# Kernel optimization log

Hardware: AMD Instinct MI355X
Metric: run time of the kernel (lower is better)

## Reference

```python
import jax, jax.numpy as jnp
import numpy as np
import math

B, S, D = 2, 2048, 512
N_BUCKETS = 64
N_HYP = int(math.log2(N_BUCKETS))  # 6


def setup_inputs() -> dict:
    key = jax.random.key(0)
    ks = jax.random.split(key, 6)
    x = jax.random.normal(ks[0], (B, S, D), dtype=jnp.float32)
    # torch.nn.Linear params: weight [out,in], bias [out]
    Wq = jax.random.normal(ks[1], (D, D), dtype=jnp.float32) / jnp.sqrt(D)
    bq = jax.random.normal(ks[2], (D,), dtype=jnp.float32) * 0.01
    Wv = jax.random.normal(ks[3], (D, D), dtype=jnp.float32) / jnp.sqrt(D)
    bv = jax.random.normal(ks[4], (D,), dtype=jnp.float32) * 0.01
    hyperplanes = jax.random.normal(ks[5], (D + 1, N_HYP), dtype=jnp.float32)
    return {"x": x, "Wq": Wq, "bq": bq, "Wv": Wv, "bv": bv, "hyperplanes": hyperplanes}


def _get_buckets(q, hyperplanes):
    # append constant-1 feature: [B,S,D+1]
    qa = jnp.concatenate([q, jnp.ones(q.shape[:2] + (1,), q.dtype)], axis=2)
    proj = jnp.einsum('bse,en->bsn', qa, hyperplanes)
    bits = (proj >= 0).astype(jnp.float32)
    powers = (2.0 ** jnp.arange(N_HYP)).astype(jnp.float32)
    return jnp.einsum('bsn,n->bs', bits, powers)  # [B,S] float bucket ids


def reference(x, Wq, bq, Wv, bv, hyperplanes):
    q = x @ Wq.T + bq
    v = x @ Wv.T + bv
    buckets = _get_buckets(q, hyperplanes)  # [B,S]
    scale = 1.0 / math.sqrt(D)

    def body(acc, i):
        # NOTE: faithful to source: tokens IN bucket i are zeroed (masked_fill
        # with mask = buckets == i), then full dense softmax attention.
        mask = (buckets == i)[..., None]  # [B,S,1]
        qb = jnp.where(mask, 0.0, q)
        vb = jnp.where(mask, 0.0, v)
        att = jax.nn.softmax(jnp.einsum('bsd,btd->bst', qb, qb) * scale, axis=-1)
        return acc + jnp.einsum('bst,btd->bsd', att, vb), None

    init = jnp.zeros_like(x)
    out, _ = jax.lax.scan(body, init, jnp.arange(N_BUCKETS, dtype=jnp.float32))
    return out
```

## Files before the change

kernel.cpp:

```cpp
#include <hip/hip_runtime.h>
#include <math.h>

#define B_ 2
#define S_ 2048
#define D_ 512
#define NB_ 64
#define NH_ 6
#define ROWS (B_*S_)
#define SCALE 0.044194173824159216f

typedef float f32x4 __attribute__((ext_vector_type(4)));
typedef __bf16 bf16v8 __attribute__((ext_vector_type(8)));
typedef short s16x8 __attribute__((ext_vector_type(8)));
typedef unsigned short u16x4 __attribute__((ext_vector_type(4)));

__device__ __forceinline__ float b2f(unsigned short u) {
    unsigned int v = (unsigned int)u << 16;
    float f; __builtin_memcpy(&f, &v, 4); return f;
}
__device__ __forceinline__ unsigned short f2b(float f) {
    unsigned int v; __builtin_memcpy(&v, &f, 4);
    v += 0x7fffu + ((v >> 16) & 1u);
    return (unsigned short)(v >> 16);
}

#define GLOAD16(g, l) __builtin_amdgcn_global_load_lds( \
    (const __attribute__((address_space(1))) unsigned int*)(g), \
    (__attribute__((address_space(3))) unsigned int*)(uintptr_t)(l), 16, 0, 0)

__device__ __forceinline__ void stage_rows(
    const unsigned short* __restrict__ src, int r0, int k0, int ld,
    unsigned short* lds, int chunk0, int nch, int l)
{
    #pragma unroll
    for (int j = 0; j < nch; ++j) {
        int chunk = chunk0 + j;
        int r = chunk * 8 + (l >> 3);
        int c = (l & 7) ^ (l >> 3);
        GLOAD16(src + (size_t)(r0 + r) * ld + k0 + c * 8, lds + chunk * 512);
    }
}

template<int EPI>
__global__ __launch_bounds__(256) void mfma_nt(
    const unsigned short* __restrict__ A, const unsigned short* __restrict__ B,
    int N, int K, long long zA, long long zB,
    float* __restrict__ Cf, long long zC,
    unsigned short* __restrict__ Ch, long long zCh,
    const float* __restrict__ e0, long long z0,
    const float* __restrict__ e1, long long z1,
    const int* __restrict__ ib, long long zi)
{
    __shared__ unsigned short Als[128 * 64];
    __shared__ unsigned short Bls[64 * 64];
    int tid = threadIdx.x;
    int w = tid >> 6, l = tid & 63;
    int wr = w >> 1, wc = w & 1;
    int zb = blockIdx.z;
    A += zb * zA;  B += zb * zB;

    int gx = gridDim.x;
    int nwg = gx * gridDim.y;
    int lin = blockIdx.y * gx + blockIdx.x;
    int qq = nwg >> 3;
    int wg = (lin & 7) * qq + (lin >> 3);
    int m0 = (wg / gx) * 128, n0 = (wg % gx) * 64;

    f32x4 acc[4][2] = {};
    int rl = l & 15, hi = l >> 4;

    for (int k0 = 0; k0 < K; k0 += 64) {
        stage_rows(A, m0, k0, K, Als, w * 4, 4, l);
        stage_rows(B, n0, k0, K, Bls, w * 2, 2, l);
        __syncthreads();
        bf16v8 af[4][2], bfr[2][2];
        const char* Ab = (const char*)Als;
        const char* Bb = (const char*)Bls;
        #pragma unroll
        for (int kk = 0; kk < 2; ++kk) {
            int kb = kk * 64 + hi * 16;
            #pragma unroll
            for (int f = 0; f < 4; ++f) {
                int ra = wr * 64 + f * 16 + rl;
                af[f][kk] = *(const bf16v8*)(Ab + ra * 128 + (kb ^ ((ra & 7) << 4)));
            }
            #pragma unroll
            for (int f = 0; f < 2; ++f) {
                int rb = wc * 32 + f * 16 + rl;
                bfr[f][kk] = *(const bf16v8*)(Bb + rb * 128 + (kb ^ ((rb & 7) << 4)));
            }
        }
        #pragma unroll
        for (int fm = 0; fm < 4; ++fm)
            #pragma unroll
            for (int fn = 0; fn < 2; ++fn)
                #pragma unroll
                for (int kk = 0; kk < 2; ++kk)
                    acc[fm][fn] = __builtin_amdgcn_mfma_f32_16x16x32_bf16(
                        af[fm][kk], bfr[fn][kk], acc[fm][fn], 0, 0, 0);
        __syncthreads();
    }

    if (EPI == 0) {
        #pragma unroll
        for (int fm = 0; fm < 4; ++fm)
            #pragma unroll
            for (int fn = 0; fn < 2; ++fn) {
                int col = n0 + wc * 32 + fn * 16 + rl;
                if (col < D_) {
                    float bs = e0[col];
                    #pragma unroll
                    for (int r = 0; r < 4; ++r) {
                        int row = m0 + wr * 64 + fm * 16 + hi * 4 + r;
                        float cv = acc[fm][fn][r] + bs;
                        Cf[(size_t)row * D_ + col] = cv;
                        Ch[(size_t)row * D_ + col] = f2b(cv);
                    }
                } else {
                    int c2 = col - D_;
                    float bs = e1[c2];
                    #pragma unroll
                    for (int r = 0; r < 4; ++r) {
                        int row = m0 + wr * 64 + fm * 16 + hi * 4 + r;
                        float cv = acc[fm][fn][r] + bs;
                        ((float*)ib)[(size_t)row * D_ + c2] = cv;
                    }
                }
            }
    } else if (EPI == 1) {
        Ch += zb * zCh;  e0 += zb * z0;
        #pragma unroll
        for (int fm = 0; fm < 4; ++fm)
            #pragma unroll
            for (int fn = 0; fn < 2; ++fn) {
                int col = n0 + wc * 32 + fn * 16 + rl;
                #pragma unroll
                for (int r = 0; r < 4; ++r) {
                    int row = m0 + wr * 64 + fm * 16 + hi * 4 + r;
                    float ev = __expf(fmaf(acc[fm][fn][r], SCALE, -e0[row]));
                    Ch[(size_t)row * N + col] = f2b(ev);
                }
            }
    } else {
        Cf += zb * zC;  e0 += zb * z0;  e1 += zb * z1;  ib += zb * zi;
        const float invS = 1.0f / (float)S_;
        #pragma unroll
        for (int fm = 0; fm < 4; ++fm)
            #pragma unroll
            for (int fn = 0; fn < 2; ++fn) {
                int col = n0 + wc * 32 + fn * 16 + rl;
                float sva = e0[col];
                #pragma unroll
                for (int r = 0; r < 4; ++r) {
                    int row = m0 + wr * 64 + fm * 16 + hi * 4 + r;
                    int bm = ib[row];
                    Cf[(size_t)row * N + col] =
                        acc[fm][fn][r] + (sva - e1[(size_t)bm * D_ + col]) * invS;
                }
            }
    }
}

__global__ void convert_bf16(const float* __restrict__ src, unsigned short* __restrict__ dst, int n)
{
    for (int i = (blockIdx.x * 256 + threadIdx.x) * 4; i < n; i += gridDim.x * 1024) {
        float4 f = *(const float4*)(src + i);
        u16x4 u = { f2b(f.x), f2b(f.y), f2b(f.z), f2b(f.w) };
        *(u16x4*)(dst + i) = u;
    }
}

__global__ __launch_bounds__(256) void transpose_v(
    const float* __restrict__ v, const int* __restrict__ perm,
    unsigned short* __restrict__ vT)
{
    __shared__ float tl[32][33];
    int b = blockIdx.z;
    int d0 = blockIdx.x * 32, s0 = blockIdx.y * 32;
    int tx = threadIdx.x & 31, ty = threadIdx.x >> 5;
    const float* vb = v + (size_t)b * S_ * D_;
    const int* pm = perm + (size_t)b * S_;
    #pragma unroll
    for (int i = 0; i < 4; ++i)
        tl[ty + i * 8][tx] = vb[(size_t)pm[s0 + ty + i * 8] * D_ + d0 + tx];
    __syncthreads();
    unsigned short* vt = vT + (size_t)b * D_ * S_;
    #pragma unroll
    for (int i = 0; i < 4; ++i)
        vt[(size_t)(d0 + ty + i * 8) * S_ + s0 + tx] = f2b(tl[tx][ty + i * 8]);
}

__global__ __launch_bounds__(64) void bucket_kernel(
    const float* __restrict__ q, const float* __restrict__ H,
    int* __restrict__ bucket, float* __restrict__ Mrow)
{
    int row = blockIdx.x;
    int lane = threadIdx.x;
    const float* qr = q + (size_t)row * D_;
    float proj[NH_] = {};
    float nrm = 0.f;
    for (int d = lane; d < D_; d += 64) {
        float qv = qr[d];
        float qb = b2f(f2b(qv));
        nrm = fmaf(qb, qb, nrm);
        #pragma unroll
        for (int n = 0; n < NH_; ++n)
            proj[n] = fmaf(qv, H[d * NH_ + n], proj[n]);
    }
    #pragma unroll
    for (int off = 32; off; off >>= 1) {
        nrm += __shfl_down(nrm, off);
        #pragma unroll
        for (int n = 0; n < NH_; ++n) proj[n] += __shfl_down(proj[n], off);
    }
    if (lane == 0) {
        int bk = 0;
        #pragma unroll
        for (int n = 0; n < NH_; ++n) {
            float p = proj[n] + H[D_ * NH_ + n];
            if (p >= 0.f) bk |= (1 << n);
        }
        bucket[row] = bk;
        Mrow[row] = nrm * SCALE;
    }
}

__global__ void zero_cnt(int* __restrict__ cnt) { cnt[threadIdx.x] = 0; }

__global__ __launch_bounds__(256) void hist_kernel(
    const int* __restrict__ bucket, int* __restrict__ cnt, int* __restrict__ idxl)
{
    int r = blockIdx.x * 256 + threadIdx.x;
    int b = r / S_;
    int s = r - b * S_;
    int j = bucket[r];
    int pos = atomicAdd(&cnt[b * NB_ + j], 1);
    idxl[((size_t)(b * NB_ + j)) * S_ + pos] = s;
}

__global__ __launch_bounds__(64) void prefix_kernel(
    const int* __restrict__ cnt, int* __restrict__ off)
{
    int b = blockIdx.x;
    int j = threadIdx.x;
    int c = cnt[b * NB_ + j];
    int x = c;
    #pragma unroll
    for (int o = 1; o < 64; o <<= 1) {
        int y = __shfl_up(x, o);
        if (j >= o) x += y;
    }
    off[b * (NB_ + 1) + j] = x - c;
    if (j == 63) off[b * (NB_ + 1) + 64] = x;
}

__global__ __launch_bounds__(64) void permbuild_kernel(
    const int* __restrict__ idxl, const int* __restrict__ cnt,
    const int* __restrict__ off, int* __restrict__ perm, int* __restrict__ p2b)
{
    int j = blockIdx.x, b = blockIdx.y;
    int n = cnt[b * NB_ + j];
    int o = off[b * (NB_ + 1) + j];
    const int* lst = idxl + ((size_t)(b * NB_ + j)) * S_;
    for (int k = threadIdx.x; k < n; k += 64) {
        perm[(size_t)b * S_ + o + k] = lst[k];
        p2b[(size_t)b * S_ + o + k] = j;
    }
}

__global__ __launch_bounds__(64) void gatherq_kernel(
    const unsigned short* __restrict__ qh, const int* __restrict__ perm,
    unsigned short* __restrict__ qp)
{
    int tp = blockIdx.x;
    int b = tp >> 11, tl = tp & (S_ - 1);
    int src = perm[(size_t)b * S_ + tl];
    const unsigned short* sp = qh + ((size_t)b * S_ + src) * D_;
    unsigned short* dp = qp + (size_t)tp * D_;
    int t = threadIdx.x * 8;
    *(s16x8*)(dp + t) = *(const s16x8*)(sp + t);
}

__global__ __launch_bounds__(256) void zwgamma_kernel(
    unsigned short* __restrict__ Eh, const int* __restrict__ p2b,
    const int* __restrict__ off, const int* __restrict__ cnt,
    const int* __restrict__ bucket, const float* __restrict__ Mrow)
{
    int row = blockIdx.x;
    int b = row >> 11;
    __shared__ float er[S_];
    __shared__ float zl[NB_];
    __shared__ float wl[NB_ + 1];
    int tid = threadIdx.x;
    unsigned short* Er = Eh + (size_t)row * S_;
    int t0 = tid * 8;
    s16x8 ev = *(const s16x8*)(Er + t0);
    #pragma unroll
    for (int i = 0; i < 8; ++i)
        er[t0 + i] = b2f((unsigned short)ev[i]);
    __syncthreads();
    {
        int j = tid >> 2, sub = tid & 3;
        int lo = off[b * (NB_ + 1) + j], hiX = off[b * (NB_ + 1) + j + 1];
        float z = 0.f;
        for (int k = lo + sub; k < hiX; k += 4) z += er[k];
        z += __shfl_xor(z, 1);
        z += __shfl_xor(z, 2);
        if (sub == 0) zl[j] = z;
    }
    __syncthreads();
    if (tid < NB_) {
        int j = tid;
        float zj = zl[j];
        float ztot = zj;
        #pragma unroll
        for (int o = 32; o; o >>= 1) ztot += __shfl_xor(ztot, o);
        int bs = bucket[row];
        float em = __expf(-Mrow[row]);
        float wj = 0.f;
        if (j != bs) wj = 1.0f / (ztot - zj + (float)cnt[b * NB_ + j] * em);
        float Wt = wj;
        #pragma unroll
        for (int o = 32; o; o >>= 1) Wt += __shfl_xor(Wt, o);
        wl[j] = wj;
        if (j == 0) wl[NB_] = Wt;
    }
    __syncthreads();
    float Wt = wl[NB_];
    const int* pb = p2b + (size_t)b * S_ + t0;
    int4 b0 = *(const int4*)pb;
    int4 b1 = *(const int4*)(pb + 4);
    s16x8 ov;
    ov[0] = (short)f2b(er[t0 + 0] * (Wt - wl[b0.x]));
    ov[1] = (short)f2b(er[t0 + 1] * (Wt - wl[b0.y]));
    ov[2] = (short)f2b(er[t0 + 2] * (Wt - wl[b0.z]));
    ov[3] = (short)f2b(er[t0 + 3] * (Wt - wl[b0.w]));
    ov[4] = (short)f2b(er[t0 + 4] * (Wt - wl[b1.x]));
    ov[5] = (short)f2b(er[t0 + 5] * (Wt - wl[b1.y]));
    ov[6] = (short)f2b(er[t0 + 6] * (Wt - wl[b1.z]));
    ov[7] = (short)f2b(er[t0 + 7] * (Wt - wl[b1.w]));
    *(s16x8*)(Er + t0) = ov;
}

__global__ __launch_bounds__(256) void sumv2_kernel(
    const float* __restrict__ v, const int* __restrict__ cnt,
    const int* __restrict__ idxl, float* __restrict__ sumVb)
{
    int j = blockIdx.x, b = blockIdx.y;
    int d = blockIdx.z * 256 + threadIdx.x;
    int n = cnt[b * NB_ + j];
    const int* lst = idxl + ((size_t)(b * NB_ + j)) * S_;
    const float* vb = v + (size_t)b * S_ * D_;
    float acc = 0.f;
    for (int k = 0; k < n; ++k)
        acc += vb[(size_t)lst[k] * D_ + d];
    sumVb[((size_t)b * NB_ + j) * D_ + d] = acc;
}

__global__ __launch_bounds__(256) void sumvall_kernel(
    const float* __restrict__ sumVb, float* __restrict__ sumVall)
{
    int b = blockIdx.y;
    int d = blockIdx.x * 256 + threadIdx.x;
    float acc = 0.f;
    for (int j = 0; j < NB_; ++j)
        acc += sumVb[((size_t)b * NB_ + j) * D_ + d];
    sumVall[b * D_ + d] = acc;
}

extern "C" void kernel_launch(void* const* d_in, const int* in_sizes, int n_in,
                              void* d_out, int out_size, void* d_ws, size_t ws_size,
                              hipStream_t stream) {
    (void)in_sizes; (void)n_in; (void)out_size; (void)ws_size;
    const float* x  = (const float*)d_in[0];
    const float* Wq = (const float*)d_in[1];
    const float* bq = (const float*)d_in[2];
    const float* Wv = (const float*)d_in[3];
    const float* bv = (const float*)d_in[4];
    const float* H  = (const float*)d_in[5];
    float* out = (float*)d_out;

    char* p = (char*)d_ws;
    auto alloc = [&](size_t bytes) -> char* {
        char* r = p; p += (bytes + 255) & ~(size_t)255; return r;
    };
    float* q       = (float*)alloc((size_t)ROWS * D_ * 4);
    float* v       = (float*)alloc((size_t)ROWS * D_ * 4);
    float* Mrow    = (float*)alloc((size_t)ROWS * 4);
    float* sumVb   = (float*)alloc((size_t)B_ * NB_ * D_ * 4);
    float* sumVall = (float*)alloc((size_t)B_ * D_ * 4);
    int*   bucket  = (int*)alloc((size_t)ROWS * 4);
    int*   cnt     = (int*)alloc((size_t)B_ * NB_ * 4);
    int*   offb    = (int*)alloc((size_t)B_ * (NB_ + 1) * 4);
    int*   perm    = (int*)alloc((size_t)B_ * S_ * 4);
    int*   p2b     = (int*)alloc((size_t)B_ * S_ * 4);
    int*   idxl    = (int*)alloc((size_t)B_ * NB_ * S_ * 4);
    unsigned short* xh   = (unsigned short*)alloc((size_t)ROWS * D_ * 2);
    unsigned short* qh   = (unsigned short*)alloc((size_t)ROWS * D_ * 2);
    unsigned short* qp   = (unsigned short*)alloc((size_t)ROWS * D_ * 2);
    unsigned short* Wqvh = (unsigned short*)alloc((size_t)2 * D_ * D_ * 2);
    unsigned short* vTh  = (unsigned short*)alloc((size_t)B_ * D_ * S_ * 2);
    unsigned short* Eh   = (unsigned short*)alloc((size_t)B_ * S_ * S_ * 2);

    convert_bf16<<<2048, 256, 0, stream>>>(x, xh, ROWS * D_);
    convert_bf16<<<256, 256, 0, stream>>>(Wq, Wqvh, D_ * D_);
    convert_bf16<<<256, 256, 0, stream>>>(Wv, Wqvh + (size_t)D_ * D_, D_ * D_);
    mfma_nt<0><<<dim3(2 * D_ / 64, ROWS / 128, 1), 256, 0, stream>>>(
        xh, Wqvh, 2 * D_, D_, 0, 0, q, 0, qh, 0, bq, 0, bv, 0, (int*)v, 0);
    bucket_kernel<<<ROWS, 64, 0, stream>>>(q, H, bucket, Mrow);
    zero_cnt<<<1, B_ * NB_, 0, stream>>>(cnt);
    hist_kernel<<<ROWS / 256, 256, 0, stream>>>(bucket, cnt, idxl);
    prefix_kernel<<<B_, 64, 0, stream>>>(cnt, offb);
    permbuild_kernel<<<dim3(NB_, B_), 64, 0, stream>>>(idxl, cnt, offb, perm, p2b);
    gatherq_kernel<<<ROWS, 64, 0, stream>>>(qh, perm, qp);
    sumv2_kernel<<<dim3(NB_, B_, D_ / 256), 256, 0, stream>>>(v, cnt, idxl, sumVb);
    sumvall_kernel<<<dim3(D_ / 256, B_), 256, 0, stream>>>(sumVb, sumVall);
    transpose_v<<<dim3(D_ / 32, S_ / 32, B_), 256, 0, stream>>>(v, perm, vTh);
    mfma_nt<1><<<dim3(S_ / 64, S_ / 128, B_), 256, 0, stream>>>(
        qh, qp, S_, D_, (long long)S_ * D_, (long long)S_ * D_,
        nullptr, 0, Eh, (long long)S_ * S_, Mrow, S_, nullptr, 0, nullptr, 0);
    zwgamma_kernel<<<ROWS, 256, 0, stream>>>(Eh, p2b, offb, cnt, bucket, Mrow);
    mfma_nt<2><<<dim3(D_ / 64, S_ / 128, B_), 256, 0, stream>>>(
        Eh, vTh, D_, S_, (long long)S_ * S_, (long long)D_ * S_,
        out, (long long)S_ * D_, nullptr, 0,
        sumVall, D_, sumVb, (long long)NB_ * D_, bucket, S_);
}
```

Baseline: 126.5 us.

## Fuse gamma scaling into PV GEMM A-load and fold row norms into projection epilogue

The zwgamma kernel no longer rewrites the S×S exp matrix in place. It now stores only per-row bucket weights (65 floats per row), and a new mfma_pv kernel applies the (Wt - w[bucket]) scaling while staging A tiles into LDS, with a 64x64 tile and an XCD-aware block swizzle. The projection GEMM epilogue also computes the squared bf16 q norms through wave reductions and atomics into Mrow, and it drops the fp32 q output. The bucket kernel now reads bf16 q. Together these remove a full read-modify-write pass over the large Eh buffer and the fp32 q traffic, at the cost of extra ALU work in the PV inner loop, atomics, and a smaller output tile.

```diff
diff --git a/kernel.cpp b/kernel.cpp
--- a/kernel.cpp
+++ b/kernel.cpp
@@ -102,32 +102,52 @@
     }
 
     if (EPI == 0) {
-        #pragma unroll
-        for (int fm = 0; fm < 4; ++fm)
-            #pragma unroll
-            for (int fn = 0; fn < 2; ++fn) {
-                int col = n0 + wc * 32 + fn * 16 + rl;
-                if (col < D_) {
+        int colBase = n0 + wc * 32;
+        if (colBase < D_) {
+            #pragma unroll
+            for (int fm = 0; fm < 4; ++fm) {
+                float p[4] = {0.f, 0.f, 0.f, 0.f};
+                #pragma unroll
+                for (int fn = 0; fn < 2; ++fn) {
+                    int col = colBase + fn * 16 + rl;
                     float bs = e0[col];
                     #pragma unroll
                     for (int r = 0; r < 4; ++r) {
                         int row = m0 + wr * 64 + fm * 16 + hi * 4 + r;
                         float cv = acc[fm][fn][r] + bs;
-                        Cf[(size_t)row * D_ + col] = cv;
-                        Ch[(size_t)row * D_ + col] = f2b(cv);
+                        unsigned short h = f2b(cv);
+                        Ch[(size_t)row * D_ + col] = h;
+                        float qb = b2f(h);
+                        p[r] = fmaf(qb, qb, p[r]);
                     }
-                } else {
-                    int c2 = col - D_;
-                    float bs = e1[c2];
+                }
+                #pragma unroll
+                for (int mask = 1; mask < 16; mask <<= 1)
+                    #pragma unroll
+                    for (int r = 0; r < 4; ++r) p[r] += __shfl_xor(p[r], mask);
+                if (rl == 0) {
                     #pragma unroll
                     for (int r = 0; r < 4; ++r) {
                         int row = m0 + wr * 64 + fm * 16 + hi * 4 + r;
-                        float cv = acc[fm][fn][r] + bs;
-                        ((float*)ib)[(size_t)row * D_ + c2] = cv;
+                        atomicAdd(&Cf[row], p[r]);
                     }
                 }
             }
-    } else if (EPI == 1) {
+        } else {
+            #pragma unroll
+            for (int fm = 0; fm < 4; ++fm)
+                #pragma unroll
+                for (int fn = 0; fn < 2; ++fn) {
+                    int col = colBase + fn * 16 + rl - D_;
+                    float bs = e1[col];
+                    #pragma unroll
+                    for (int r = 0; r < 4; ++r) {
+                        int row = m0 + wr * 64 + fm * 16 + hi * 4 + r;
+                        ((float*)ib)[(size_t)row * D_ + col] = acc[fm][fn][r] + bs;
+                    }
+                }
+        }
+    } else {
         Ch += zb * zCh;  e0 += zb * z0;
         #pragma unroll
         for (int fm = 0; fm < 4; ++fm)
@@ -141,24 +161,117 @@
                     Ch[(size_t)row * N + col] = f2b(ev);
                 }
             }
-    } else {
-        Cf += zb * zC;  e0 += zb * z0;  e1 += zb * z1;  ib += zb * zi;
-        const float invS = 1.0f / (float)S_;
-        #pragma unroll
-        for (int fm = 0; fm < 4; ++fm)
-            #pragma unroll
-            for (int fn = 0; fn < 2; ++fn) {
-                int col = n0 + wc * 32 + fn * 16 + rl;
-                float sva = e0[col];
-                #pragma unroll
-                for (int r = 0; r < 4; ++r) {
-                    int row = m0 + wr * 64 + fm * 16 + hi * 4 + r;
-                    int bm = ib[row];
-                    Cf[(size_t)row * N + col] =
-                        acc[fm][fn][r] + (sva - e1[(size_t)bm * D_ + col]) * invS;
-                }
-            }
-    }
+    }
+}
+
+__global__ __launch_bounds__(256) void mfma_pv(
+    const unsigned short* __restrict__ Eh, const unsigned short* __restrict__ vT,
+    const float* __restrict__ wl, const int* __restrict__ p2b,
+    const float* __restrict__ sumVall, const float* __restrict__ sumVb,
+    const int* __restrict__ bucket, float* __restrict__ out)
+{
+    __shared__ unsigned short Als[64 * 64];
+    __shared__ unsigned short Bls[64 * 64];
+    int tid = threadIdx.x, w = tid >> 6, l = tid & 63;
+    int wr = w >> 1, wc = w & 1, rl = l & 15, hi = l >> 4;
+    int zb = blockIdx.z;
+    const unsigned short* A  = Eh + (size_t)zb * S_ * S_;
+    const unsigned short* Bv = vT + (size_t)zb * D_ * S_;
+    const float* wlb = wl + (size_t)zb * S_ * 65;
+    const int* pb = p2b + (size_t)zb * S_;
+    const float* sva = sumVall + (size_t)zb * D_;
+    const float* svb = sumVb + (size_t)zb * NB_ * D_;
+    const int* bkt = bucket + (size_t)zb * S_;
+    float* outb = out + (size_t)zb * S_ * D_;
+
+    int lin = blockIdx.y * 8 + blockIdx.x;
+    int xcd = lin & 7, pos = lin >> 3;
+    int m0 = (xcd * 4 + (pos >> 3)) * 64;
+    int n0 = (pos & 7) * 64;
+
+    int rA[2]; float wtA[2];
+    #pragma unroll
+    for (int j = 0; j < 2; ++j) {
+        rA[j] = (w * 2 + j) * 8 + (l >> 3);
+        wtA[j] = wlb[(size_t)(m0 + rA[j]) * 65 + 64];
+    }
+    int cA = l & 7;
+
+    f32x4 acc[2][2] = {};
+    for (int k0 = 0; k0 < S_; k0 += 64) {
+        #pragma unroll
+        for (int j = 0; j < 2; ++j) {
+            int r = rA[j];
+            int row = m0 + r;
+            int t = k0 + cA * 8;
+            s16x8 g = *(const s16x8*)(A + (size_t)row * S_ + t);
+            int4 pb0 = *(const int4*)(pb + t);
+            int4 pb1 = *(const int4*)(pb + t + 4);
+            const float* wrp = wlb + (size_t)row * 65;
+            float wt = wtA[j];
+            s16x8 o;
+            if (pb0.x == pb1.w) {
+                float g1 = wt - wrp[pb0.x];
+                #pragma unroll
+                for (int i = 0; i < 8; ++i)
+                    o[i] = (short)f2b(b2f((unsigned short)g[i]) * g1);
+            } else {
+                int bb[8] = {pb0.x, pb0.y, pb0.z, pb0.w, pb1.x, pb1.y, pb1.z, pb1.w};
+                #pragma unroll
+                for (int i = 0; i < 8; ++i)
+                    o[i] = (short)f2b(b2f((unsigned short)g[i]) * (wt - wrp[bb[i]]));
+            }
+            int dst = r * 128 + ((cA * 16) ^ ((r & 7) << 4));
+            *(s16x8*)((char*)Als + dst) = o;
+        }
+        stage_rows(Bv, n0, k0, S_, Bls, w * 2, 2, l);
+        __syncthreads();
+        bf16v8 af[2][2], bfr[2][2];
+        const char* Ab = (const char*)Als;
+        const char* Bb = (const char*)Bls;
+        #pragma unroll
+        for (int kk = 0; kk < 2; ++kk) {
+            int kb = kk * 64 + hi * 16;
+            #pragma unroll
+            for (int f = 0; f < 2; ++f) {
+                int ra = wr * 32 + f * 16 + rl;
+                af[f][kk] = *(const bf16v8*)(Ab + ra * 128 + (kb ^ ((ra & 7) << 4)));
+                int rb = wc * 32 + f * 16 + rl;
+                bfr[f][kk] = *(const bf16v8*)(Bb + rb * 128 + (kb ^ ((rb & 7) << 4)));
+            }
+        }
+        #pragma unroll
+        for (int fm = 0; fm < 2; ++fm)
+            #pragma unroll
+            for (int fn = 0; fn < 2; ++fn)
+                #pragma unroll
+                for (int kk = 0; kk < 2; ++kk)
+                    acc[fm][fn] = __builtin_amdgcn_mfma_f32_16x16x32_bf16(
+                        af[fm][kk], bfr[fn][kk], acc[fm][fn], 0, 0, 0);
+        __syncthreads();
+    }
+    const float invS = 1.0f / (float)S_;
+    #pragma unroll
+    for (int fm = 0; fm < 2; ++fm)
+        #pragma unroll
+        for (int fn = 0; fn < 2; ++fn) {
+            int col = n0 + wc * 32 + fn * 16 + rl;
+            float sa = sva[col];
+            #pragma unroll
+            for (int r = 0; r < 4; ++r) {
+                int row = m0 + wr * 32 + fm * 16 + hi * 4 + r;
+                int bm = bkt[row];
+                outb[(size_t)row * D_ + col] =
+                    acc[fm][fn][r] + (sa - svb[(size_t)bm * D_ + col]) * invS;
+            }
+        }
+}
+
+__global__ void init_kernel(float* __restrict__ Mrow, int* __restrict__ cnt)
+{
+    int i = blockIdx.x * 256 + threadIdx.x;
+    if (i < ROWS) Mrow[i] = 0.f;
+    if (i < B_ * NB_) cnt[i] = 0;
 }
 
 __global__ void convert_bf16(const float* __restrict__ src, unsigned short* __restrict__ dst, int n)
@@ -191,25 +304,21 @@
 }
 
 __global__ __launch_bounds__(64) void bucket_kernel(
-    const float* __restrict__ q, const float* __restrict__ H,
+    const unsigned short* __restrict__ qh, const float* __restrict__ H,
     int* __restrict__ bucket, float* __restrict__ Mrow)
 {
     int row = blockIdx.x;
     int lane = threadIdx.x;
-    const float* qr = q + (size_t)row * D_;
+    const unsigned short* qr = qh + (size_t)row * D_;
     float proj[NH_] = {};
-    float nrm = 0.f;
     for (int d = lane; d < D_; d += 64) {
-        float qv = qr[d];
-        float qb = b2f(f2b(qv));
-        nrm = fmaf(qb, qb, nrm);
+        float qv = b2f(qr[d]);
         #pragma unroll
         for (int n = 0; n < NH_; ++n)
             proj[n] = fmaf(qv, H[d * NH_ + n], proj[n]);
     }
     #pragma unroll
     for (int off = 32; off; off >>= 1) {
-        nrm += __shfl_down(nrm, off);
         #pragma unroll
         for (int n = 0; n < NH_; ++n) proj[n] += __shfl_down(proj[n], off);
     }
@@ -221,11 +330,9 @@
             if (p >= 0.f) bk |= (1 << n);
         }
         bucket[row] = bk;
-        Mrow[row] = nrm * SCALE;
-    }
-}
-
-__global__ void zero_cnt(int* __restrict__ cnt) { cnt[threadIdx.x] = 0; }
+        Mrow[row] = Mrow[row] * SCALE;
+    }
+}
 
 __global__ __launch_bounds__(256) void hist_kernel(
     const int* __restrict__ bucket, int* __restrict__ cnt, int* __restrict__ idxl)
@@ -281,18 +388,17 @@
     *(s16x8*)(dp + t) = *(const s16x8*)(sp + t);
 }
 
-__global__ __launch_bounds__(256) void zwgamma_kernel(
-    unsigned short* __restrict__ Eh, const int* __restrict__ p2b,
-    const int* __restrict__ off, const int* __restrict__ cnt,
-    const int* __restrict__ bucket, const float* __restrict__ Mrow)
+__global__ __launch_bounds__(256) void zw_kernel(
+    const unsigned short* __restrict__ Eh, const int* __restrict__ off,
+    const int* __restrict__ cnt, const int* __restrict__ bucket,
+    const float* __restrict__ Mrow, float* __restrict__ wl)
 {
     int row = blockIdx.x;
     int b = row >> 11;
     __shared__ float er[S_];
     __shared__ float zl[NB_];
-    __shared__ float wl[NB_ + 1];
     int tid = threadIdx.x;
-    unsigned short* Er = Eh + (size_t)row * S_;
+    const unsigned short* Er = Eh + (size_t)row * S_;
     int t0 = tid * 8;
     s16x8 ev = *(const s16x8*)(Er + t0);
     #pragma unroll
@@ -322,24 +428,9 @@
         float Wt = wj;
         #pragma unroll
         for (int o = 32; o; o >>= 1) Wt += __shfl_xor(Wt, o);
-        wl[j] = wj;
-        if (j == 0) wl[NB_] = Wt;
-    }
-    __syncthreads();
-    float Wt = wl[NB_];
-    const int* pb = p2b + (size_t)b * S_ + t0;
-    int4 b0 = *(const int4*)pb;
-    int4 b1 = *(const int4*)(pb + 4);
-    s16x8 ov;
-    ov[0] = (short)f2b(er[t0 + 0] * (Wt - wl[b0.x]));
-    ov[1] = (short)f2b(er[t0 + 1] * (Wt - wl[b0.y]));
-    ov[2] = (short)f2b(er[t0 + 2] * (Wt - wl[b0.z]));
-    ov[3] = (short)f2b(er[t0 + 3] * (Wt - wl[b0.w]));
-    ov[4] = (short)f2b(er[t0 + 4] * (Wt - wl[b1.x]));
-    ov[5] = (short)f2b(er[t0 + 5] * (Wt - wl[b1.y]));
-    ov[6] = (short)f2b(er[t0 + 6] * (Wt - wl[b1.z]));
-    ov[7] = (short)f2b(er[t0 + 7] * (Wt - wl[b1.w]));
-    *(s16x8*)(Er + t0) = ov;
+        wl[(size_t)row * 65 + j] = wj;
+        if (j == 0) wl[(size_t)row * 65 + 64] = Wt;
+    }
 }
 
 __global__ __launch_bounds__(256) void sumv2_kernel(
@@ -384,9 +475,9 @@
     auto alloc = [&](size_t bytes) -> char* {
         char* r = p; p += (bytes + 255) & ~(size_t)255; return r;
     };
-    float* q       = (float*)alloc((size_t)ROWS * D_ * 4);
     float* v       = (float*)alloc((size_t)ROWS * D_ * 4);
     float* Mrow    = (float*)alloc((size_t)ROWS * 4);
+    float* wl      = (float*)alloc((size_t)ROWS * 65 * 4);
     float* sumVb   = (float*)alloc((size_t)B_ * NB_ * D_ * 4);
     float* sumVall = (float*)alloc((size_t)B_ * D_ * 4);
     int*   bucket  = (int*)alloc((size_t)ROWS * 4);
@@ -402,13 +493,13 @@
     unsigned short* vTh  = (unsigned short*)alloc((size_t)B_ * D_ * S_ * 2);
     unsigned short* Eh   = (unsigned short*)alloc((size_t)B_ * S_ * S_ * 2);
 
+    init_kernel<<<ROWS / 256, 256, 0, stream>>>(Mrow, cnt);
     convert_bf16<<<2048, 256, 0, stream>>>(x, xh, ROWS * D_);
     convert_bf16<<<256, 256, 0, stream>>>(Wq, Wqvh, D_ * D_);
     convert_bf16<<<256, 256, 0, stream>>>(Wv, Wqvh + (size_t)D_ * D_, D_ * D_);
     mfma_nt<0><<<dim3(2 * D_ / 64, ROWS / 128, 1), 256, 0, stream>>>(
-        xh, Wqvh, 2 * D_, D_, 0, 0, q, 0, qh, 0, bq, 0, bv, 0, (int*)v, 0);
-    bucket_kernel<<<ROWS, 64, 0, stream>>>(q, H, bucket, Mrow);
-    zero_cnt<<<1, B_ * NB_, 0, stream>>>(cnt);
+        xh, Wqvh, 2 * D_, D_, 0, 0, Mrow, 0, qh, 0, bq, 0, bv, 0, (int*)v, 0);
+    bucket_kernel<<<ROWS, 64, 0, stream>>>(qh, H, bucket, Mrow);
     hist_kernel<<<ROWS / 256, 256, 0, stream>>>(bucket, cnt, idxl);
     prefix_kernel<<<B_, 64, 0, stream>>>(cnt, offb);
     permbuild_kernel<<<dim3(NB_, B_), 64, 0, stream>>>(idxl, cnt, offb, perm, p2b);
@@ -419,9 +510,7 @@
     mfma_nt<1><<<dim3(S_ / 64, S_ / 128, B_), 256, 0, stream>>>(
         qh, qp, S_, D_, (long long)S_ * D_, (long long)S_ * D_,
         nullptr, 0, Eh, (long long)S_ * S_, Mrow, S_, nullptr, 0, nullptr, 0);
-    zwgamma_kernel<<<ROWS, 256, 0, stream>>>(Eh, p2b, offb, cnt, bucket, Mrow);
-    mfma_nt<2><<<dim3(D_ / 64, S_ / 128, B_), 256, 0, stream>>>(
-        Eh, vTh, D_, S_, (long long)S_ * S_, (long long)D_ * S_,
-        out, (long long)S_ * D_, nullptr, 0,
-        sumVall, D_, sumVb, (long long)NB_ * D_, bucket, S_);
-}
+    zw_kernel<<<ROWS, 256, 0, stream>>>(Eh, offb, cnt, bucket, Mrow, wl);
+    mfma_pv<<<dim3(D_ / 64, S_ / 64, B_), 256, 0, stream>>>(
+        Eh, vTh, wl, p2b, sumVall, sumVb, bucket, out);
+}
```

Measured after the change: 177.9 us. 40.6% more time.
